# Kernel optimization log

Measured on AMD Instinct MI355X. Metric: run time of the kernel, lower is better.

The kernel has to match this reference:

```python
import jax, jax.numpy as jnp
import numpy as np

N, IN, H, OUT, C = 1024, 64, 64, 64, 32
EPS = 1e-5   # SAKELayer.epsilon
INF = 1e5    # SAKELayer.inf


def _w(key, i, o, scale=1.0):
    return jax.random.normal(key, (i, o), jnp.float32) * (scale / np.sqrt(i))


def setup_inputs() -> dict:
    key = jax.random.key(0)
    ks = jax.random.split(key, 16)
    return dict(
        h=jax.random.normal(ks[0], (N, IN), jnp.float32),
        x=jax.random.normal(ks[1], (N, 3), jnp.float32),
        # edge model (ConcatenationFilter): Linear(2*IN+1,H), SiLU, Linear(H,H)
        ew1=_w(ks[2], 2 * IN + 1, H), eb1=jnp.zeros((H,), jnp.float32),
        ew2=_w(ks[3], H, H), eb2=jnp.zeros((H,), jnp.float32),
        # node_mlp: Linear(2H+IN,H), SiLU, Linear(H,OUT)
        nw1=_w(ks[4], 2 * H + IN, H), nb1=jnp.zeros((H,), jnp.float32),
        nw2=_w(ks[5], H, OUT), nb2=jnp.zeros((OUT,), jnp.float32),
        # coordinate_mlp: Linear(H,H), SiLU, Linear(H,1,bias=False) xavier gain 1e-3
        cw1=_w(ks[6], H, H), cb1=jnp.zeros((H,), jnp.float32),
        cw2=_w(ks[7], H, 1, scale=1e-3),
        # semantic_attention_mlp: Linear(H,1), LeakyReLU
        aw=_w(ks[8], H, 1), ab=jnp.zeros((1,), jnp.float32),
        # coefficients_mlp: Linear(H,H), SiLU, Linear(H,C)
        fw1=_w(ks[9], H, H), fb1=jnp.zeros((H,), jnp.float32),
        fw2=_w(ks[10], H, C), fb2=jnp.zeros((C,), jnp.float32),
        # post_norm_mlp: Linear(C,H), SiLU, Linear(H,H)
        pw1=_w(ks[11], C, H), pb1=jnp.zeros((H,), jnp.float32),
        pw2=_w(ks[12], H, H), pb2=jnp.zeros((H,), jnp.float32),
        log_gamma=jnp.array(0.0, jnp.float32),
    )


def reference(h, x, ew1, eb1, ew2, eb2, nw1, nb1, nw2, nb2, cw1, cb1, cw2,
              aw, ab, fw1, fb1, fw2, fb2, pw1, pb1, pw2, pb2, log_gamma):
    n, d_in = h.shape
    silu = jax.nn.silu
    eye = jnp.eye(n, dtype=h.dtype)[:, :, None]                    # [n,n,1]

    x_minus_xt = x[:, None, :] - x[None, :, :]                     # [n,n,3]
    norm = jnp.sqrt(jnp.sum(x_minus_xt ** 2, -1, keepdims=True) + EPS)  # [n,n,1]

    h_cat_ht = jnp.concatenate(
        [jnp.broadcast_to(h[:, None, :], (n, n, d_in)),
         jnp.broadcast_to(h[None, :, :], (n, n, d_in))], -1)       # [n,n,2*IN]

    # edge model: MLP over concat(features, distance)
    e_in = jnp.concatenate([h_cat_ht, norm], -1)                   # [n,n,2*IN+1]
    h_e = silu(e_in @ ew1 + eb1) @ ew2 + eb2                       # [n,n,H]

    # euclidean attention over neighbors j (diag masked by +INF distance)
    att_e = jax.nn.softmax(-(norm + INF * eye) * jnp.exp(log_gamma), axis=1)
    # semantic attention
    att_s = jax.nn.softmax(jax.nn.leaky_relu(h_e @ aw + ab) - INF * eye, axis=1)
    comb = att_e * att_s
    comb = comb / (jnp.sum(comb, axis=1, keepdims=True) + EPS)     # [n,n,1]
    h_e_att = h_e * comb                                           # [n,n,H]

    # spatial attention: equivariant coefficient combinations
    coeff = silu(h_e_att @ fw1 + fb1) @ fw2 + fb2                  # [n,n,C]
    dirs = x_minus_xt / (norm + 1.0)                               # [n,n,3]
    combos = jnp.einsum('ijc,ijd->icd', coeff, dirs) / n           # mean over j -> [n,C,3]
    h_comb = silu(jnp.sum(combos ** 2, -1) @ pw1 + pb1) @ pw2 + pb2  # [n,H]

    # node update
    h_agg = jnp.sum(h_e_att, axis=1)                               # [n,H]
    node_in = jnp.concatenate([h, h_agg, h_comb], -1)              # [n,2H+IN]
    h_out = h + (silu(node_in @ nw1 + nb1) @ nw2 + nb2)            # residual

    # equivariant coordinate update
    phi = silu(h_e @ cw1 + cb1) @ cw2                              # [n,n,1]
    x_out = x + jnp.mean(x_minus_xt * phi, axis=1)                 # [n,3]
    return h_out, x_out
```

## Files before the change

### kernel.cpp

```cpp
#include <hip/hip_runtime.h>
#include <hip/hip_bf16.h>

#define NN 1024
#define LSTR 72
#define EPSV 1e-5f
#define BIGINF 1e5f

typedef __attribute__((ext_vector_type(8))) short short8;
typedef __attribute__((ext_vector_type(4))) short short4v;
typedef __attribute__((ext_vector_type(4))) float f32x4;

__device__ __forceinline__ float siluf(float v) {
    return v * __builtin_amdgcn_rcpf(1.0f + __expf(-v));
}
__device__ __forceinline__ float pnorm(float dx, float dy, float dz) {
    return sqrtf(dx * dx + dy * dy + dz * dz + EPSV);
}
__device__ __forceinline__ float wsum(float v) {
#pragma unroll
    for (int off = 32; off > 0; off >>= 1) v += __shfl_xor(v, off, 64);
    return v;
}
__device__ __forceinline__ float redquad(float v) {
    v += __shfl_xor(v, 16, 64); v += __shfl_xor(v, 32, 64);
    return v;
}
__device__ __forceinline__ short f2bs(float v) {
    __hip_bfloat16 b = __float2bfloat16(v);
    return *reinterpret_cast<short*>(&b);
}
__device__ __forceinline__ short f2bt(float v) {
    return (short)(__float_as_uint(v) >> 16);
}

__global__ void kA(const float* __restrict__ h, const float* __restrict__ ew1,
                   const float* __restrict__ eb1, const float* __restrict__ ew2,
                   const float* __restrict__ cw1, const float* __restrict__ fw1,
                   const float* __restrict__ fw2, const float* __restrict__ aw,
                   const float* __restrict__ ab, const float* __restrict__ eb2,
                   float* __restrict__ HA, float* __restrict__ HB,
                   float* __restrict__ HBT, short* __restrict__ ew2T,
                   short* __restrict__ cw1T, short* __restrict__ fw1T,
                   short* __restrict__ fw2T, float* __restrict__ wsv,
                   float* __restrict__ svb) {
    const int b = blockIdx.x;
    const int o = threadIdx.x;
    if (b < NN) {
        const int i = b;
        float hv = h[i * 64 + o];
        float a = 0.f, bb = eb1[o];
#pragma unroll
        for (int k = 0; k < 64; k++) {
            float hk = __shfl(hv, k, 64);
            a += hk * ew1[k * 64 + o];
            bb += hk * ew1[(64 + k) * 64 + o];
        }
        HA[i * 64 + o] = a;
        HB[i * 64 + o] = bb;
        HBT[o * NN + i] = bb;
    } else if (b < NN + 64) {
        const int r = b - NN;
        ew2T[r * 64 + o] = f2bs(ew2[o * 64 + r]);
        cw1T[r * 64 + o] = f2bs(cw1[o * 64 + r]);
        fw1T[r * 64 + o] = f2bs(fw1[o * 64 + r]);
        if (r < 32) fw2T[r * 64 + o] = f2bs(fw2[o * 32 + r]);
    } else {
        float s = 0.f;
#pragma unroll
        for (int q = 0; q < 64; q++) s += ew2[o * 64 + q] * aw[q];
        wsv[o] = s;
        float e = wsum(eb2[o] * aw[o]);
        if (o == 0) svb[0] = e + ab[0];
    }
}

__global__ __launch_bounds__(256) void kBn(
    const float* __restrict__ x, const float* __restrict__ ew1,
    const float* __restrict__ HA, const float* __restrict__ HBT,
    const float* __restrict__ wsv, const float* __restrict__ svb,
    const float* __restrict__ lg, float* __restrict__ ls,
    float* __restrict__ rowm, float* __restrict__ rowd) {
    const int i = blockIdx.x;
    const int t = threadIdx.x;
    const float* HAi = HA + i * 64;
    const float* w1 = ew1 + 128 * 64;
    const float gamma = __expf(lg[0]);
    const float svb0 = svb[0];
    const float xi0 = x[i * 3 + 0], xi1 = x[i * 3 + 1], xi2 = x[i * 3 + 2];

    float4 xa = ((const float4*)x)[3 * t + 0];
    float4 xb = ((const float4*)x)[3 * t + 1];
    float4 xc = ((const float4*)x)[3 * t + 2];
    float nrm[4], le[4], lv[4];
    {
        float dx0 = xi0 - xa.x, dy0 = xi1 - xa.y, dz0 = xi2 - xa.z;
        float dx1 = xi0 - xa.w, dy1 = xi1 - xb.x, dz1 = xi2 - xb.y;
        float dx2 = xi0 - xb.z, dy2 = xi1 - xb.w, dz2 = xi2 - xc.x;
        float dx3 = xi0 - xc.y, dy3 = xi1 - xc.z, dz3 = xi2 - xc.w;
        nrm[0] = pnorm(dx0, dy0, dz0);
        nrm[1] = pnorm(dx1, dy1, dz1);
        nrm[2] = pnorm(dx2, dy2, dz2);
        nrm[3] = pnorm(dx3, dy3, dz3);
    }
    float d0 = 0.f, d1 = 0.f, d2 = 0.f, d3 = 0.f;
#pragma unroll 8
    for (int k = 0; k < 64; k++) {
        float4 hb = *(const float4*)&HBT[k * NN + 4 * t];
        float hk = HAi[k], w1k = w1[k], wv = wsv[k];
        d0 += siluf(hk + hb.x + nrm[0] * w1k) * wv;
        d1 += siluf(hk + hb.y + nrm[1] * w1k) * wv;
        d2 += siluf(hk + hb.z + nrm[2] * w1k) * wv;
        d3 += siluf(hk + hb.w + nrm[3] * w1k) * wv;
    }
    float me = -3.0e38f, ms = -3.0e38f;
    float4 svo;
    {
        float dd[4] = {d0, d1, d2, d3};
#pragma unroll
        for (int m = 0; m < 4; m++) {
            int j = 4 * t + m;
            float sv = dd[m] + svb0;
            sv = sv >= 0.f ? sv : 0.01f * sv;
            if (j == i) sv -= BIGINF;
            lv[m] = sv;
            le[m] = -(nrm[m] + (j == i ? BIGINF : 0.f)) * gamma;
            me = fmaxf(me, le[m]);
            ms = fmaxf(ms, lv[m]);
        }
        svo.x = lv[0]; svo.y = lv[1]; svo.z = lv[2]; svo.w = lv[3];
    }
    *(float4*)&ls[(size_t)i * NN + 4 * t] = svo;

    __shared__ float sm[4], ss[4], s1[4], s2[4], s3[4];
#pragma unroll
    for (int off = 32; off > 0; off >>= 1) {
        me = fmaxf(me, __shfl_xor(me, off, 64));
        ms = fmaxf(ms, __shfl_xor(ms, off, 64));
    }
    const int w = t >> 6;
    if ((t & 63) == 0) { sm[w] = me; ss[w] = ms; }
    __syncthreads();
    me = fmaxf(fmaxf(sm[0], sm[1]), fmaxf(sm[2], sm[3]));
    ms = fmaxf(fmaxf(ss[0], ss[1]), fmaxf(ss[2], ss[3]));
    float Se = 0.f, Ss = 0.f, Sq = 0.f;
#pragma unroll
    for (int m = 0; m < 4; m++) {
        float ee = __expf(le[m] - me);
        float es = __expf(lv[m] - ms);
        Se += ee; Ss += es; Sq += ee * es;
    }
    Se = wsum(Se); Ss = wsum(Ss); Sq = wsum(Sq);
    if ((t & 63) == 0) { s1[w] = Se; s2[w] = Ss; s3[w] = Sq; }
    __syncthreads();
    if (t == 0) {
        rowm[i] = me + ms;
        rowd[i] = (s3[0] + s3[1] + s3[2] + s3[3]) +
                  EPSV * (s1[0] + s1[1] + s1[2] + s1[3]) * (s2[0] + s2[1] + s2[2] + s2[3]);
    }
}

__device__ __forceinline__ void stageW(const short* __restrict__ g, short* s,
                                       int tid, int rows) {
    for (int c = tid; c < rows * 16; c += 512) {
        int r = c >> 4, q = c & 15;
        *(short4v*)&s[r * LSTR + q * 4] = *(const short4v*)&g[r * 64 + q * 4];
    }
}

__global__ __launch_bounds__(512) void kD(
    const float* __restrict__ x, const float* __restrict__ ew1,
    const float* __restrict__ eb2, const float* __restrict__ cb1,
    const float* __restrict__ fb1, const float* __restrict__ lg,
    const float* __restrict__ HA, const float* __restrict__ HB,
    const short* __restrict__ ew2T, const short* __restrict__ cw1T,
    const short* __restrict__ fw1T,
    const float* __restrict__ ls, const float* __restrict__ rowm,
    const float* __restrict__ rowd, float* __restrict__ hagg,
    float* __restrict__ Gw, float* __restrict__ H2w, float* __restrict__ sdw) {
    __shared__ __align__(16) short sWe[64 * LSTR];
    __shared__ __align__(16) short sWf[64 * LSTR];
    __shared__ __align__(16) short sScr[8][16 * LSTR];
    __shared__ float sHag[64], sG[192], sH2[192], sSd[3];

    const int tid = threadIdx.x;
    const int i = blockIdx.x;
    const int lane = tid & 63, w = tid >> 6;
    const int col = lane & 15, quad = lane >> 4;

    stageW(ew2T, sWe, tid, 64);
    stageW(fw1T, sWf, tid, 64);
    if (tid < 64) sHag[tid] = 0.f;
    else if (tid < 256) sG[tid - 64] = 0.f;
    else if (tid < 448) sH2[tid - 256] = 0.f;
    else if (tid < 451) sSd[tid - 448] = 0.f;

    short* scr = sScr[w];
    const float gamma = __expf(lg[0]);

    float eb[4], cbv[4], fbv[4];
#pragma unroll
    for (int nb = 0; nb < 4; nb++) {
        eb[nb] = eb2[nb * 16 + col];
        cbv[nb] = cb1[nb * 16 + col];
        fbv[nb] = fb1[nb * 16 + col];
    }
    const float rm = rowm[i];
    const float invd = 1.0f / rowd[i];
    const float xi0 = x[i * 3 + 0], xi1 = x[i * 3 + 1], xi2 = x[i * 3 + 2];
    const float* lsi = ls + (size_t)i * NN;

    float hagA[4] = {0.f, 0.f, 0.f, 0.f};
    float Ga[12]  = {0.f, 0.f, 0.f, 0.f, 0.f, 0.f, 0.f, 0.f, 0.f, 0.f, 0.f, 0.f};
    float H2a[12] = {0.f, 0.f, 0.f, 0.f, 0.f, 0.f, 0.f, 0.f, 0.f, 0.f, 0.f, 0.f};
    float sdx = 0.f, sdy = 0.f, sdz = 0.f;
    __syncthreads();

#pragma unroll 1
    for (int jt = 0; jt < 8; jt++) {
        const int r = jt * 128 + w * 16 + col;
        float dx = xi0 - x[r * 3 + 0], dy = xi1 - x[r * 3 + 1], dz = xi2 - x[r * 3 + 2];
        float nr = pnorm(dx, dy, dz);
        float iv = __builtin_amdgcn_rcpf(nr + 1.0f);
        sdx += dx * iv; sdy += dy * iv; sdz += dz * iv;
        float le = -(nr + (r == i ? BIGINF : 0.f)) * gamma;
        float cb = __expf(le + lsi[r] - rm) * invd;

        short8 af[2];
#pragma unroll
        for (int kb = 0; kb < 2; kb++) {
            const float* hA = &HA[i * 64 + kb * 32 + quad * 8];
            const float* wr = &ew1[128 * 64 + kb * 32 + quad * 8];
            const float* hb = &HB[r * 64 + kb * 32 + quad * 8];
#pragma unroll
            for (int t = 0; t < 8; t++)
                af[kb][t] = f2bt(siluf(hA[t] + hb[t] + nr * wr[t]));
        }
        f32x4 ac[4] = {{0.f,0.f,0.f,0.f},{0.f,0.f,0.f,0.f},{0.f,0.f,0.f,0.f},{0.f,0.f,0.f,0.f}};
#pragma unroll
        for (int kb = 0; kb < 2; kb++) {
#pragma unroll
            for (int nb = 0; nb < 4; nb++) {
                short8 b = *(const short8*)&sWe[(nb * 16 + col) * LSTR + kb * 32 + quad * 8];
                ac[nb] = __builtin_amdgcn_mfma_f32_16x16x32_bf16(af[kb], b, ac[nb], 0, 0, 0);
            }
        }
        float cm[4];
#pragma unroll
        for (int reg = 0; reg < 4; reg++) cm[reg] = __shfl(cb, quad * 4 + reg, 64);
#pragma unroll
        for (int nb = 0; nb < 4; nb++) {
#pragma unroll
            for (int reg = 0; reg < 4; reg++) {
                float h0 = ac[nb][reg] + eb[nb];
                scr[(quad * 4 + reg) * LSTR + nb * 16 + col] = f2bt(h0);
                hagA[nb] += h0 * cm[reg];
            }
        }
        short8 a0 = *(const short8*)&scr[col * LSTR + quad * 8];
        short8 a1 = *(const short8*)&scr[col * LSTR + 32 + quad * 8];

        {
            f32x4 p[4] = {{0.f,0.f,0.f,0.f},{0.f,0.f,0.f,0.f},{0.f,0.f,0.f,0.f},{0.f,0.f,0.f,0.f}};
#pragma unroll
            for (int nb = 0; nb < 4; nb++) {
                short8 b0 = *(const short8*)&cw1T[(nb * 16 + col) * 64 + quad * 8];
                short8 b1 = *(const short8*)&cw1T[(nb * 16 + col) * 64 + 32 + quad * 8];
                p[nb] = __builtin_amdgcn_mfma_f32_16x16x32_bf16(a0, b0, p[nb], 0, 0, 0);
                p[nb] = __builtin_amdgcn_mfma_f32_16x16x32_bf16(a1, b1, p[nb], 0, 0, 0);
            }
#pragma unroll
            for (int reg = 0; reg < 4; reg++) {
                int sl = quad * 4 + reg;
                float tx = __shfl(dx, sl, 64), ty = __shfl(dy, sl, 64), tz = __shfl(dz, sl, 64);
#pragma unroll
                for (int nb = 0; nb < 4; nb++) {
                    float s0 = siluf(p[nb][reg] + cbv[nb]);
                    H2a[nb * 3 + 0] += s0 * tx;
                    H2a[nb * 3 + 1] += s0 * ty;
                    H2a[nb * 3 + 2] += s0 * tz;
                }
            }
        }

        {
            f32x4 v[4] = {{0.f,0.f,0.f,0.f},{0.f,0.f,0.f,0.f},{0.f,0.f,0.f,0.f},{0.f,0.f,0.f,0.f}};
#pragma unroll
            for (int nb = 0; nb < 4; nb++) {
                short8 b0 = *(const short8*)&sWf[(nb * 16 + col) * LSTR + quad * 8];
                short8 b1 = *(const short8*)&sWf[(nb * 16 + col) * LSTR + 32 + quad * 8];
                v[nb] = __builtin_amdgcn_mfma_f32_16x16x32_bf16(a0, b0, v[nb], 0, 0, 0);
                v[nb] = __builtin_amdgcn_mfma_f32_16x16x32_bf16(a1, b1, v[nb], 0, 0, 0);
            }
#pragma unroll
            for (int reg = 0; reg < 4; reg++) {
                int sl = quad * 4 + reg;
                float ti = __shfl(iv, sl, 64);
                float fx = __shfl(dx, sl, 64) * ti;
                float fy = __shfl(dy, sl, 64) * ti;
                float fz = __shfl(dz, sl, 64) * ti;
#pragma unroll
                for (int nb = 0; nb < 4; nb++) {
                    float w0 = siluf(cm[reg] * v[nb][reg] + fbv[nb]);
                    Ga[nb * 3 + 0] += w0 * fx;
                    Ga[nb * 3 + 1] += w0 * fy;
                    Ga[nb * 3 + 2] += w0 * fz;
                }
            }
        }
    }

#pragma unroll
    for (int nb = 0; nb < 4; nb++) {
        float v = redquad(hagA[nb]);
        if (quad == 0) atomicAdd(&sHag[nb * 16 + col], v);
    }
#pragma unroll
    for (int nb = 0; nb < 4; nb++) {
#pragma unroll
        for (int d = 0; d < 3; d++) {
            float v = redquad(H2a[nb * 3 + d]);
            if (quad == 0) atomicAdd(&sH2[(nb * 16 + col) * 3 + d], v);
            float g = redquad(Ga[nb * 3 + d]);
            if (quad == 0) atomicAdd(&sG[(nb * 16 + col) * 3 + d], g);
        }
    }
    sdx = wsum(sdx); sdy = wsum(sdy); sdz = wsum(sdz);
    if (lane == 0) {
        atomicAdd(&sSd[0], 0.25f * sdx);
        atomicAdd(&sSd[1], 0.25f * sdy);
        atomicAdd(&sSd[2], 0.25f * sdz);
    }
    __syncthreads();
    if (tid < 64) hagg[i * 64 + tid] = sHag[tid];
    else if (tid < 256) Gw[i * 192 + tid - 64] = sG[tid - 64];
    else if (tid < 448) H2w[i * 192 + tid - 256] = sH2[tid - 256];
    else if (tid < 451) sdw[i * 3 + tid - 448] = sSd[tid - 448];
}

__global__ void kE(const float* __restrict__ h, const float* __restrict__ x,
                   const float* __restrict__ nw1, const float* __restrict__ nb1,
                   const float* __restrict__ nw2, const float* __restrict__ nb2,
                   const float* __restrict__ pw1, const float* __restrict__ pb1,
                   const float* __restrict__ pw2, const float* __restrict__ pb2,
                   const float* __restrict__ fw2, const float* __restrict__ fb2,
                   const float* __restrict__ cw2,
                   const float* __restrict__ hagg, const float* __restrict__ Gw,
                   const float* __restrict__ H2w, const float* __restrict__ sdw,
                   float* __restrict__ out) {
    const int i = blockIdx.x, o = threadIdx.x;
    const float invN = 1.0f / (float)NN;
    float cw2o = cw2[o];
    float xd0 = wsum(cw2o * H2w[i * 192 + o * 3 + 0]);
    float xd1 = wsum(cw2o * H2w[i * 192 + o * 3 + 1]);
    float xd2 = wsum(cw2o * H2w[i * 192 + o * 3 + 2]);
    float g0 = Gw[i * 192 + o * 3 + 0];
    float g1 = Gw[i * 192 + o * 3 + 1];
    float g2 = Gw[i * 192 + o * 3 + 2];
    float v0 = 0.f, v1 = 0.f, v2 = 0.f;
#pragma unroll
    for (int m = 0; m < 64; m++) {
        float fw = fw2[m * 32 + (o & 31)];
        v0 += __shfl(g0, m, 64) * fw;
        v1 += __shfl(g1, m, 64) * fw;
        v2 += __shfl(g2, m, 64) * fw;
    }
    float r = 0.f;
    if (o < 32) {
        float fb = fb2[o];
        float u0 = (v0 + fb * sdw[i * 3 + 0]) * invN;
        float u1 = (v1 + fb * sdw[i * 3 + 1]) * invN;
        float u2 = (v2 + fb * sdw[i * 3 + 2]) * invN;
        r = u0 * u0 + u1 * u1 + u2 * u2;
    }
    float t1 = pb1[o];
#pragma unroll
    for (int k = 0; k < 32; k++) t1 += __shfl(r, k, 64) * pw1[k * 64 + o];
    t1 = siluf(t1);
    float hc = pb2[o];
#pragma unroll
    for (int k = 0; k < 64; k++) hc += __shfl(t1, k, 64) * pw2[k * 64 + o];
    float hi = h[i * 64 + o];
    float ha = hagg[i * 64 + o];
    float t2 = nb1[o];
#pragma unroll
    for (int k = 0; k < 64; k++) t2 += __shfl(hi, k, 64) * nw1[k * 64 + o];
#pragma unroll
    for (int k = 0; k < 64; k++) t2 += __shfl(ha, k, 64) * nw1[(64 + k) * 64 + o];
#pragma unroll
    for (int k = 0; k < 64; k++) t2 += __shfl(hc, k, 64) * nw1[(128 + k) * 64 + o];
    t2 = siluf(t2);
    float ho = hi + nb2[o];
#pragma unroll
    for (int k = 0; k < 64; k++) ho += __shfl(t2, k, 64) * nw2[k * 64 + o];
    out[i * 64 + o] = ho;
    if (o < 3) {
        float xdv = o == 0 ? xd0 : (o == 1 ? xd1 : xd2);
        out[NN * 64 + i * 3 + o] = x[i * 3 + o] + xdv * invN;
    }
}

extern "C" void kernel_launch(void* const* d_in, const int* in_sizes, int n_in,
                              void* d_out, int out_size, void* d_ws, size_t ws_size,
                              hipStream_t stream) {
    (void)in_sizes; (void)n_in; (void)out_size; (void)ws_size;
    const float* h   = (const float*)d_in[0];
    const float* x   = (const float*)d_in[1];
    const float* ew1 = (const float*)d_in[2];
    const float* eb1 = (const float*)d_in[3];
    const float* ew2 = (const float*)d_in[4];
    const float* eb2 = (const float*)d_in[5];
    const float* nw1 = (const float*)d_in[6];
    const float* nb1 = (const float*)d_in[7];
    const float* nw2 = (const float*)d_in[8];
    const float* nb2 = (const float*)d_in[9];
    const float* cw1 = (const float*)d_in[10];
    const float* cb1 = (const float*)d_in[11];
    const float* cw2 = (const float*)d_in[12];
    const float* aw  = (const float*)d_in[13];
    const float* ab  = (const float*)d_in[14];
    const float* fw1 = (const float*)d_in[15];
    const float* fb1 = (const float*)d_in[16];
    const float* fw2 = (const float*)d_in[17];
    const float* fb2 = (const float*)d_in[18];
    const float* pw1 = (const float*)d_in[19];
    const float* pb1 = (const float*)d_in[20];
    const float* pw2 = (const float*)d_in[21];
    const float* pb2 = (const float*)d_in[22];
    const float* lg  = (const float*)d_in[23];
    float* out = (float*)d_out;

    float* W      = (float*)d_ws;
    float* ls     = W;
    float* HA     = ls + (size_t)NN * NN;
    float* HB     = HA + NN * 64;
    float* HBT    = HB + NN * 64;
    float* rowm   = HBT + NN * 64;
    float* rowd   = rowm + NN;
    float* hagg   = rowd + NN;
    float* combos = hagg + NN * 64;
    float* xupd   = combos + NN * 96;
    float* wsv    = xupd + NN * 3;
    float* svb    = wsv + 64;
    short* ew2T   = (short*)(svb + 4);
    short* cw1T   = ew2T + 64 * 64;
    short* fw1T   = cw1T + 64 * 64;
    short* fw2T   = fw1T + 64 * 64;
    float* Gw     = (float*)(fw2T + 32 * 64);
    float* H2w    = Gw + (size_t)NN * 192;
    float* sdw    = H2w + (size_t)NN * 192;

    kA<<<NN + 65, 64, 0, stream>>>(h, ew1, eb1, ew2, cw1, fw1, fw2, aw, ab, eb2,
                                   HA, HB, HBT, ew2T, cw1T, fw1T, fw2T, wsv, svb);
    kBn<<<NN, 256, 0, stream>>>(x, ew1, HA, HBT, wsv, svb, lg, ls, rowm, rowd);
    kD<<<NN, 512, 0, stream>>>(x, ew1, eb2, cb1, fb1, lg, HA, HB,
                               ew2T, cw1T, fw1T, ls, rowm, rowd,
                               hagg, Gw, H2w, sdw);
    kE<<<NN, 64, 0, stream>>>(h, x, nw1, nb1, nw2, nb2, pw1, pb1, pw2, pb2,
                              fw2, fb2, cw2, hagg, Gw, H2w, sdw, out);
}
```

Measured before the change: 283.0 us.

## Stage cw1 in LDS and fold fw2/cw2 reductions into kD epilogue

The cw1 weight tile is now copied into shared memory once per block, so the inner MFMA loop no longer reads it from global memory on every iteration. The final fw2 and cw2 contractions move out of kE into kD's epilogue, where they read directly from the shared accumulators. As a result kD writes only compact combos and xupd vectors, and the 192-wide Gw and H2w intermediates disappear. This costs extra LDS per block, which may lower occupancy, and adds a serial 64-term loop on a few threads at the end of kD.

```diff
diff --git a/kernel.cpp b/kernel.cpp
--- a/kernel.cpp
+++ b/kernel.cpp
@@ -171,14 +171,17 @@
     const float* __restrict__ x, const float* __restrict__ ew1,
     const float* __restrict__ eb2, const float* __restrict__ cb1,
     const float* __restrict__ fb1, const float* __restrict__ lg,
+    const float* __restrict__ fw2, const float* __restrict__ fb2,
+    const float* __restrict__ cw2,
     const float* __restrict__ HA, const float* __restrict__ HB,
     const short* __restrict__ ew2T, const short* __restrict__ cw1T,
     const short* __restrict__ fw1T,
     const float* __restrict__ ls, const float* __restrict__ rowm,
     const float* __restrict__ rowd, float* __restrict__ hagg,
-    float* __restrict__ Gw, float* __restrict__ H2w, float* __restrict__ sdw) {
+    float* __restrict__ combos, float* __restrict__ xupd) {
     __shared__ __align__(16) short sWe[64 * LSTR];
     __shared__ __align__(16) short sWf[64 * LSTR];
+    __shared__ __align__(16) short sWc[64 * LSTR];
     __shared__ __align__(16) short sScr[8][16 * LSTR];
     __shared__ float sHag[64], sG[192], sH2[192], sSd[3];
 
@@ -189,6 +192,7 @@
 
     stageW(ew2T, sWe, tid, 64);
     stageW(fw1T, sWf, tid, 64);
+    stageW(cw1T, sWc, tid, 64);
     if (tid < 64) sHag[tid] = 0.f;
     else if (tid < 256) sG[tid - 64] = 0.f;
     else if (tid < 448) sH2[tid - 256] = 0.f;
@@ -263,8 +267,8 @@
             f32x4 p[4] = {{0.f,0.f,0.f,0.f},{0.f,0.f,0.f,0.f},{0.f,0.f,0.f,0.f},{0.f,0.f,0.f,0.f}};
 #pragma unroll
             for (int nb = 0; nb < 4; nb++) {
-                short8 b0 = *(const short8*)&cw1T[(nb * 16 + col) * 64 + quad * 8];
-                short8 b1 = *(const short8*)&cw1T[(nb * 16 + col) * 64 + 32 + quad * 8];
+                short8 b0 = *(const short8*)&sWc[(nb * 16 + col) * LSTR + quad * 8];
+                short8 b1 = *(const short8*)&sWc[(nb * 16 + col) * LSTR + 32 + quad * 8];
                 p[nb] = __builtin_amdgcn_mfma_f32_16x16x32_bf16(a0, b0, p[nb], 0, 0, 0);
                 p[nb] = __builtin_amdgcn_mfma_f32_16x16x32_bf16(a1, b1, p[nb], 0, 0, 0);
             }
@@ -331,10 +335,24 @@
         atomicAdd(&sSd[2], 0.25f * sdz);
     }
     __syncthreads();
-    if (tid < 64) hagg[i * 64 + tid] = sHag[tid];
-    else if (tid < 256) Gw[i * 192 + tid - 64] = sG[tid - 64];
-    else if (tid < 448) H2w[i * 192 + tid - 256] = sH2[tid - 256];
-    else if (tid < 451) sdw[i * 3 + tid - 448] = sSd[tid - 448];
+
+    if (tid < 128) {
+        int c = tid >> 2, d = tid & 3;
+        if (d < 3) {
+            float acc = fb2[c] * sSd[d];
+#pragma unroll
+            for (int m = 0; m < 64; m++) acc += fw2[m * 32 + c] * sG[m * 3 + d];
+            combos[i * 96 + c * 3 + d] = acc;
+        }
+    } else if (tid < 131) {
+        int d = tid - 128;
+        float acc = 0.f;
+#pragma unroll
+        for (int n = 0; n < 64; n++) acc += cw2[n] * sH2[n * 3 + d];
+        xupd[i * 3 + d] = acc;
+    } else if (tid >= 192 && tid < 256) {
+        hagg[i * 64 + tid - 192] = sHag[tid - 192];
+    }
 }
 
 __global__ void kE(const float* __restrict__ h, const float* __restrict__ x,
@@ -342,35 +360,16 @@
                    const float* __restrict__ nw2, const float* __restrict__ nb2,
                    const float* __restrict__ pw1, const float* __restrict__ pb1,
                    const float* __restrict__ pw2, const float* __restrict__ pb2,
-                   const float* __restrict__ fw2, const float* __restrict__ fb2,
-                   const float* __restrict__ cw2,
-                   const float* __restrict__ hagg, const float* __restrict__ Gw,
-                   const float* __restrict__ H2w, const float* __restrict__ sdw,
-                   float* __restrict__ out) {
+                   const float* __restrict__ hagg, const float* __restrict__ combos,
+                   const float* __restrict__ xupd, float* __restrict__ out) {
     const int i = blockIdx.x, o = threadIdx.x;
     const float invN = 1.0f / (float)NN;
-    float cw2o = cw2[o];
-    float xd0 = wsum(cw2o * H2w[i * 192 + o * 3 + 0]);
-    float xd1 = wsum(cw2o * H2w[i * 192 + o * 3 + 1]);
-    float xd2 = wsum(cw2o * H2w[i * 192 + o * 3 + 2]);
-    float g0 = Gw[i * 192 + o * 3 + 0];
-    float g1 = Gw[i * 192 + o * 3 + 1];
-    float g2 = Gw[i * 192 + o * 3 + 2];
-    float v0 = 0.f, v1 = 0.f, v2 = 0.f;
-#pragma unroll
-    for (int m = 0; m < 64; m++) {
-        float fw = fw2[m * 32 + (o & 31)];
-        v0 += __shfl(g0, m, 64) * fw;
-        v1 += __shfl(g1, m, 64) * fw;
-        v2 += __shfl(g2, m, 64) * fw;
-    }
     float r = 0.f;
     if (o < 32) {
-        float fb = fb2[o];
-        float u0 = (v0 + fb * sdw[i * 3 + 0]) * invN;
-        float u1 = (v1 + fb * sdw[i * 3 + 1]) * invN;
-        float u2 = (v2 + fb * sdw[i * 3 + 2]) * invN;
-        r = u0 * u0 + u1 * u1 + u2 * u2;
+        float v0 = combos[i * 96 + o * 3 + 0] * invN;
+        float v1 = combos[i * 96 + o * 3 + 1] * invN;
+        float v2 = combos[i * 96 + o * 3 + 2] * invN;
+        r = v0 * v0 + v1 * v1 + v2 * v2;
     }
     float t1 = pb1[o];
 #pragma unroll
@@ -393,10 +392,8 @@
 #pragma unroll
     for (int k = 0; k < 64; k++) ho += __shfl(t2, k, 64) * nw2[k * 64 + o];
     out[i * 64 + o] = ho;
-    if (o < 3) {
-        float xdv = o == 0 ? xd0 : (o == 1 ? xd1 : xd2);
-        out[NN * 64 + i * 3 + o] = x[i * 3 + o] + xdv * invN;
-    }
+    if (o < 3)
+        out[NN * 64 + i * 3 + o] = x[i * 3 + o] + xupd[i * 3 + o] * invN;
 }
 
 extern "C" void kernel_launch(void* const* d_in, const int* in_sizes, int n_in,
@@ -445,16 +442,13 @@
     short* cw1T   = ew2T + 64 * 64;
     short* fw1T   = cw1T + 64 * 64;
     short* fw2T   = fw1T + 64 * 64;
-    float* Gw     = (float*)(fw2T + 32 * 64);
-    float* H2w    = Gw + (size_t)NN * 192;
-    float* sdw    = H2w + (size_t)NN * 192;
 
     kA<<<NN + 65, 64, 0, stream>>>(h, ew1, eb1, ew2, cw1, fw1, fw2, aw, ab, eb2,
                                    HA, HB, HBT, ew2T, cw1T, fw1T, fw2T, wsv, svb);
     kBn<<<NN, 256, 0, stream>>>(x, ew1, HA, HBT, wsv, svb, lg, ls, rowm, rowd);
-    kD<<<NN, 512, 0, stream>>>(x, ew1, eb2, cb1, fb1, lg, HA, HB,
-                               ew2T, cw1T, fw1T, ls, rowm, rowd,
-                               hagg, Gw, H2w, sdw);
+    kD<<<NN, 512, 0, stream>>>(x, ew1, eb2, cb1, fb1, lg, fw2, fb2, cw2,
+                               HA, HB, ew2T, cw1T, fw1T, ls, rowm, rowd,
+                               hagg, combos, xupd);
     kE<<<NN, 64, 0, stream>>>(h, x, nw1, nb1, nw2, nb2, pw1, pb1, pw2, pb2,
-                              fw2, fb2, cw2, hagg, Gw, H2w, sdw, out);
-}
+                              hagg, combos, xupd, out);
+}
```

New measurement: 257.7 us, median of 2. 1.1x faster.
